# Kernel tuning notes

Hardware: AMD Instinct MI355X
Metric: run time of the kernel (lower is better)

The kernel has to match this reference:

```python
import jax, jax.numpy as jnp
import numpy as np

N, E, G = 50000, 640000, 256
NODE_IN, EDGE_IN, H, L, T = 64, 16, 128, 4, 5
BN_EPS = 1e-5

def setup_inputs() -> dict:
    key = jax.random.key(0)
    ks = jax.random.split(key, 24)
    s = lambda k, shape, fan: jax.random.normal(k, shape, jnp.float32) * (1.0 / np.sqrt(fan))
    return {
        "x": jax.random.normal(ks[0], (N, NODE_IN), jnp.float32),
        "edge_attr": jax.random.normal(ks[1], (E, EDGE_IN), jnp.float32),
        "node_w": s(ks[2], (NODE_IN, H), NODE_IN), "node_b": jnp.zeros((H,), jnp.float32),
        "edge_w1": s(ks[3], (EDGE_IN, H), EDGE_IN), "edge_b1": jnp.zeros((H,), jnp.float32),
        "edge_w2": s(ks[4], (H, H), H), "edge_b2": jnp.zeros((H,), jnp.float32),
        "conv_w1": s(ks[5], (L, H, H), H), "conv_b1": jnp.zeros((L, H), jnp.float32),
        "conv_w2": s(ks[6], (L, H, H), H), "conv_b2": jnp.zeros((L, H), jnp.float32),
        "bn_gamma": jnp.ones((L, H), jnp.float32), "bn_beta": jnp.zeros((L, H), jnp.float32),
        "gate_w1": s(ks[7], (H, H // 2), H), "gate_b1": jnp.zeros((H // 2,), jnp.float32),
        "gate_w2": s(ks[8], (H // 2, 1), H // 2), "gate_b2": jnp.zeros((1,), jnp.float32),
        "head_w1": s(ks[9], (H, H), H), "head_b1": jnp.zeros((H,), jnp.float32),
        "head_w2": s(ks[10], (H, T), H), "head_b2": jnp.zeros((T,), jnp.float32),
        "edge_index": jax.random.randint(ks[11], (2, E), 0, N, jnp.int32),
        "batch": jnp.sort(jax.random.randint(ks[12], (N,), 0, G, jnp.int32)),
    }

def reference(x, edge_attr, node_w, node_b, edge_w1, edge_b1, edge_w2, edge_b2,
              conv_w1, conv_b1, conv_w2, conv_b2, bn_gamma, bn_beta,
              gate_w1, gate_b1, gate_w2, gate_b2, head_w1, head_b1, head_w2, head_b2,
              edge_index, batch):
    relu = jax.nn.relu
    h = x @ node_w + node_b                                   # [N,H]
    e = relu(edge_attr @ edge_w1 + edge_b1) @ edge_w2 + edge_b2  # [E,H]
    src, dst = edge_index[0], edge_index[1]
    bn_scale = 1.0 / jnp.sqrt(jnp.float32(1.0) + BN_EPS)      # eval BN: mean=0, var=1
    for l in range(L):
        m = relu(h[src] + e)                                  # GINEConv message [E,H]
        aggr = jax.ops.segment_sum(m, dst, num_segments=N)    # scatter-add
        z = h + aggr                                          # eps=0: (1+eps)*x + aggr
        z = relu(z @ conv_w1[l] + conv_b1[l]) @ conv_w2[l] + conv_b2[l]
        z = z * bn_scale * bn_gamma[l] + bn_beta[l]
        h = relu(z)                                           # dropout off (eval)
    gate = relu(h @ gate_w1 + gate_b1) @ gate_w2 + gate_b2    # [N,1]
    gmax = jax.ops.segment_max(gate, batch, num_segments=G)   # segment softmax
    wexp = jnp.exp(gate - gmax[batch])
    denom = jax.ops.segment_sum(wexp, batch, num_segments=G)
    alpha = wexp / denom[batch]
    g = jax.ops.segment_sum(alpha * h, batch, num_segments=G) # [G,H]
    return relu(g @ head_w1 + head_b1) @ head_w2 + head_b2    # [G,T]
```

## Files before the change

kernel.cpp:

```cpp
#include <hip/hip_runtime.h>

typedef unsigned short u16;
typedef __bf16 bf16x8 __attribute__((ext_vector_type(8)));
typedef float f32x4 __attribute__((ext_vector_type(4)));
typedef unsigned short u16x8 __attribute__((ext_vector_type(8)));

#define NNODES 50000
#define NEDGES 640000
#define NGRAPH 256

__device__ __forceinline__ float bf2f(u16 u) {
  unsigned int v = ((unsigned int)u) << 16; float f; __builtin_memcpy(&f, &v, 4); return f;
}
__device__ __forceinline__ u16 f2bf(float f) {
  unsigned int x; __builtin_memcpy(&x, &f, 4);
  unsigned int lsb = (x >> 16) & 1u;
  x += 0x7fffu + lsb;
  return (u16)(x >> 16);
}

__global__ void write_zero_f32(float* __restrict__ out, int n) {
  int i = blockIdx.x * 256 + threadIdx.x;
  if (i < n) out[i] = 0.f;
}

__global__ void zero_counts(int* __restrict__ a, int na, int* __restrict__ b, int nb) {
  int i = blockIdx.x * 256 + threadIdx.x;
  if (i < na) a[i] = 0;
  if (i < nb) b[i] = 0;
}

__global__ void prep_weights(const float* __restrict__ node_w, const float* __restrict__ edge_w1,
                             const float* __restrict__ edge_w2, const float* __restrict__ conv_w1,
                             const float* __restrict__ conv_w2, const float* __restrict__ gate_w1,
                             u16* __restrict__ node_wt, u16* __restrict__ edge_w1t,
                             u16* __restrict__ edge_w2t, u16* __restrict__ conv_w1t,
                             u16* __restrict__ conv_w2t, u16* __restrict__ gate_w1t) {
  int o = blockIdx.x * 256 + threadIdx.x;
  if (o < 8192) { int n = o >> 6, k = o & 63; node_wt[o] = f2bf(node_w[k * 128 + n]); return; }
  o -= 8192;
  if (o < 4096) { int n = o >> 5, k = o & 31;
                  edge_w1t[o] = (k < 16) ? f2bf(edge_w1[k * 128 + n]) : (u16)0; return; }
  o -= 4096;
  if (o < 16384) { int n = o >> 7, k = o & 127; edge_w2t[o] = f2bf(edge_w2[k * 128 + n]); return; }
  o -= 16384;
  if (o < 65536) { int l = o >> 14, r = o & 16383, n = r >> 7, k = r & 127;
                   conv_w1t[o] = f2bf(conv_w1[l * 16384 + k * 128 + n]); return; }
  o -= 65536;
  if (o < 65536) { int l = o >> 14, r = o & 16383, n = r >> 7, k = r & 127;
                   conv_w2t[o] = f2bf(conv_w2[l * 16384 + k * 128 + n]); return; }
  o -= 65536;
  if (o < 8192) { int n = o >> 7, k = o & 127; gate_w1t[o] = f2bf(gate_w1[k * 64 + n]); }
}

__global__ void hist_all(const int* __restrict__ dst, const int* __restrict__ b,
                         int* __restrict__ counts, int* __restrict__ gc, int n) {
  int i = blockIdx.x * 256 + threadIdx.x;
  atomicAdd(&counts[dst[i]], 1);
  if (i < n) atomicAdd(&gc[b[i]], 1);
}
__global__ void scan_a(const int* __restrict__ counts, int* __restrict__ bsums, int n) {
  int b = blockIdx.x, t = threadIdx.x;
  int i0 = b * 1024 + t * 4;
  int s = 0;
#pragma unroll
  for (int j = 0; j < 4; j++) { int i = i0 + j; if (i < n) s += counts[i]; }
  int lane = t & 63, w = t >> 6;
  for (int m = 32; m; m >>= 1) s += __shfl_xor(s, m, 64);
  __shared__ int ws_[4];
  if (lane == 0) ws_[w] = s;
  __syncthreads();
  if (t == 0) bsums[b] = ws_[0] + ws_[1] + ws_[2] + ws_[3];
}
__global__ void scan_b(int* __restrict__ bsums, int* __restrict__ offs, int nb, int n) {
  if (threadIdx.x == 0) {
    int run = 0;
    for (int i = 0; i < nb; i++) { int v = bsums[i]; bsums[i] = run; run += v; }
    offs[n] = run;
  }
}
__global__ void scan_c(const int* __restrict__ counts, const int* __restrict__ boffs,
                       int* __restrict__ offs, int* __restrict__ cursor, int n) {
  int b = blockIdx.x, t = threadIdx.x;
  int i0 = b * 1024 + t * 4;
  int v[4]; int s = 0;
#pragma unroll
  for (int j = 0; j < 4; j++) { v[j] = (i0 + j < n) ? counts[i0 + j] : 0; s += v[j]; }
  int lane = t & 63, w = t >> 6;
  int x = s;
  for (int d = 1; d < 64; d <<= 1) { int y = __shfl_up(x, (unsigned)d, 64); if (lane >= d) x += y; }
  __shared__ int wt_[4];
  if (lane == 63) wt_[w] = x;
  __syncthreads();
  int add = boffs[b];
  for (int i = 0; i < w; i++) add += wt_[i];
  int excl = add + x - s;
#pragma unroll
  for (int j = 0; j < 4; j++) {
    int i = i0 + j;
    if (i < n) { offs[i] = excl; cursor[i] = excl; }
    excl += v[j];
  }
}
__global__ void gscan(const int* __restrict__ gcounts, int* __restrict__ goffs) {
  int t = threadIdx.x;
  int v = gcounts[t];
  int lane = t & 63, w = t >> 6;
  int x = v;
  for (int d = 1; d < 64; d <<= 1) { int y = __shfl_up(x, (unsigned)d, 64); if (lane >= d) x += y; }
  __shared__ int wt_[4];
  if (lane == 63) wt_[w] = x;
  __syncthreads();
  int add = 0;
  for (int i = 0; i < w; i++) add += wt_[i];
  int incl = add + x;
  goffs[t] = incl - v;
  if (t == 255) goffs[256] = incl;
}
__global__ void scatter_csr(const int* __restrict__ src, const int* __restrict__ dst,
                            int* __restrict__ cursor, int* __restrict__ csr_src,
                            int* __restrict__ csr_eid) {
  int i = blockIdx.x * 256 + threadIdx.x;
  int d = dst[i];
  int p = atomicAdd(&cursor[d], 1);
  csr_src[p] = src[i];
  csr_eid[p] = i;
}

template <int KB, int SA, int SB>
__device__ __forceinline__ void mfma_block(const u16* aL, const u16* bL, int m, int quad,
                                           int rbase, f32x4* acc) {
#pragma unroll
  for (int kb = 0; kb < KB; ++kb) {
    bf16x8 a = *(const bf16x8*)(aL + (rbase + m) * SA + kb * 32 + quad * 8);
#pragma unroll
    for (int nt = 0; nt < 8; ++nt) {
      bf16x8 b = *(const bf16x8*)(bL + (nt * 16 + m) * SB + kb * 32 + quad * 8);
      acc[nt] = __builtin_amdgcn_mfma_f32_16x16x32_bf16(a, b, acc[nt], 0, 0, 0);
    }
  }
}

__global__ __launch_bounds__(256) void node_encode(const float* __restrict__ x,
                                                   const u16* __restrict__ wt,
                                                   const float* __restrict__ nb,
                                                   u16* __restrict__ hb, int n) {
  __shared__ alignas(16) u16 sA[64 * 72];
  __shared__ alignas(16) u16 sW[128 * 72];
  int t = threadIdx.x;
  int row0 = blockIdx.x * 64;
#pragma unroll
  for (int i = 0; i < 4; i++) {
    int idx = t + 256 * i; int r = idx >> 4, c = idx & 15;
    int grow = row0 + r; if (grow > n - 1) grow = n - 1;
    float4 v = *(const float4*)(x + (size_t)grow * 64 + c * 4);
    ushort4 o; o.x = f2bf(v.x); o.y = f2bf(v.y); o.z = f2bf(v.z); o.w = f2bf(v.w);
    *(ushort4*)&sA[r * 72 + c * 4] = o;
  }
#pragma unroll
  for (int i = 0; i < 4; i++) {
    int idx = t + 256 * i; int nr = idx >> 3, c = idx & 7;
    *(uint4*)&sW[nr * 72 + c * 8] = *(const uint4*)(wt + nr * 64 + c * 8);
  }
  __syncthreads();
  int lane = t & 63, w = t >> 6, m = lane & 15, quad = lane >> 4, rbase = w * 16;
  f32x4 acc[8];
  f32x4 z4 = {0.f, 0.f, 0.f, 0.f};
#pragma unroll
  for (int i = 0; i < 8; i++) acc[i] = z4;
  mfma_block<2, 72, 72>(sA, sW, m, quad, rbase, acc);
#pragma unroll
  for (int nt = 0; nt < 8; nt++) {
    int col = nt * 16 + m;
    float bb = nb[col];
    f32x4 a4 = acc[nt];
#pragma unroll
    for (int r = 0; r < 4; r++) {
      int grow = row0 + rbase + quad * 4 + r;
      if (grow < n) hb[(size_t)grow * 128 + col] = f2bf(a4[r] + bb);
    }
  }
}

__global__ __launch_bounds__(256) void edge_encode(const float* __restrict__ ea,
                                                   const u16* __restrict__ w1t,
                                                   const u16* __restrict__ w2t,
                                                   const float* __restrict__ b1,
                                                   const float* __restrict__ b2,
                                                   const int* __restrict__ csr_eid,
                                                   u16* __restrict__ e_perm) {
  __shared__ alignas(16) u16 sA[64 * 48];
  __shared__ alignas(16) u16 sMid[64 * 136];
  int t = threadIdx.x;
  int lane = t & 63, w = t >> 6, m = lane & 15, quad = lane >> 4, rbase = w * 16;
  int s0 = blockIdx.x * 64;

  if (t < 128) {
    int r = t >> 1, c = t & 1;
    uint4 z = {0, 0, 0, 0};
    *(uint4*)&sA[r * 48 + 16 + c * 8] = z;
  }
  {
    int eidv = 0;
    if (lane < 16) eidv = csr_eid[s0 + w * 16 + lane];
    int r = lane >> 2, c = lane & 3;
    int eid = __shfl(eidv, r, 64);
    float4 v = *(const float4*)(ea + (size_t)eid * 16 + c * 4);
    ushort4 o; o.x = f2bf(v.x); o.y = f2bf(v.y); o.z = f2bf(v.z); o.w = f2bf(v.w);
    *(ushort4*)&sA[(w * 16 + r) * 48 + c * 4] = o;
  }
  bf16x8 w1f[8];
  float b1r[8];
#pragma unroll
  for (int nt = 0; nt < 8; nt++) {
    w1f[nt] = *(const bf16x8*)(w1t + (nt * 16 + m) * 32 + quad * 8);
    b1r[nt] = b1[nt * 16 + m];
  }
  __syncthreads();

  f32x4 z4 = {0.f, 0.f, 0.f, 0.f};
  f32x4 acc[8];
#pragma unroll
  for (int i = 0; i < 8; i++) acc[i] = z4;
  {
    bf16x8 a = *(const bf16x8*)(&sA[(rbase + m) * 48 + quad * 8]);
#pragma unroll
    for (int nt = 0; nt < 8; nt++)
      acc[nt] = __builtin_amdgcn_mfma_f32_16x16x32_bf16(a, w1f[nt], acc[nt], 0, 0, 0);
  }
#pragma unroll
  for (int nt = 0; nt < 8; nt++) {
#pragma unroll
    for (int r = 0; r < 4; r++) {
      float v = fmaxf(acc[nt][r] + b1r[nt], 0.f);
      unsigned int lo = f2bf(v);
      unsigned int hi = __shfl_xor(lo, 1, 64);
      if ((m & 1) == 0) {
        int rr = rbase + quad * 4 + r;
        *(unsigned int*)&sMid[rr * 136 + nt * 16 + m] = lo | (hi << 16);
      }
    }
  }
  bf16x8 w2f[8];
  float4 b2v[2];
#pragma unroll
  for (int ct = 0; ct < 2; ct++) {
    b2v[ct] = *(const float4*)&b2[w * 32 + ct * 16 + quad * 4];
#pragma unroll
    for (int kb = 0; kb < 4; kb++)
      w2f[ct * 4 + kb] = *(const bf16x8*)(w2t + (size_t)(w * 32 + ct * 16 + m) * 128 + kb * 32 + quad * 8);
  }
  __syncthreads();

  f32x4 acc2[8];
#pragma unroll
  for (int i = 0; i < 8; i++) acc2[i] = z4;
#pragma unroll
  for (int rt = 0; rt < 4; rt++) {
#pragma unroll
    for (int kb = 0; kb < 4; kb++) {
      bf16x8 a = *(const bf16x8*)(&sMid[(rt * 16 + m) * 136 + kb * 32 + quad * 8]);
      acc2[rt * 2 + 0] = __builtin_amdgcn_mfma_f32_16x16x32_bf16(w2f[kb], a, acc2[rt * 2 + 0], 0, 0, 0);
      acc2[rt * 2 + 1] = __builtin_amdgcn_mfma_f32_16x16x32_bf16(w2f[4 + kb], a, acc2[rt * 2 + 1], 0, 0, 0);
    }
  }
#pragma unroll
  for (int rt = 0; rt < 4; rt++) {
#pragma unroll
    for (int ct = 0; ct < 2; ct++) {
      f32x4 a4 = acc2[rt * 2 + ct];
      u16 q0 = f2bf(a4[0] + b2v[ct].x);
      u16 q1 = f2bf(a4[1] + b2v[ct].y);
      u16 q2 = f2bf(a4[2] + b2v[ct].z);
      u16 q3 = f2bf(a4[3] + b2v[ct].w);
      uint2 pk;
      pk.x = (unsigned int)q0 | ((unsigned int)q1 << 16);
      pk.y = (unsigned int)q2 | ((unsigned int)q3 << 16);
      *(uint2*)(e_perm + (size_t)(s0 + rt * 16 + m) * 128 + w * 32 + ct * 16 + quad * 4) = pk;
    }
  }
}

__global__ __launch_bounds__(256) void aggregate_k(const u16* __restrict__ hb,
                                                   const u16* __restrict__ e_perm,
                                                   const int* __restrict__ offs,
                                                   const int* __restrict__ csr_src,
                                                   u16* __restrict__ z, int n) {
  int node = blockIdx.x * 4 + (threadIdx.x >> 6);
  if (node >= n) return;
  int lane = threadIdx.x & 63;
  int q = lane >> 4, li = lane & 15;
  int s0 = offs[node], s1 = offs[node + 1];
  float a[8];
#pragma unroll
  for (int j = 0; j < 8; j++) a[j] = 0.f;
  int s = s0 + q;
  for (; s + 8 <= s1; s += 8) {
    int v0 = csr_src[s], v1 = csr_src[s + 4];
    u16x8 h0 = *(const u16x8*)(hb + (size_t)v0 * 128 + li * 8);
    u16x8 e0 = *(const u16x8*)(e_perm + (size_t)s * 128 + li * 8);
    u16x8 h1 = *(const u16x8*)(hb + (size_t)v1 * 128 + li * 8);
    u16x8 e1 = *(const u16x8*)(e_perm + (size_t)(s + 4) * 128 + li * 8);
#pragma unroll
    for (int j = 0; j < 8; j++) {
      a[j] += fmaxf(bf2f(h0[j]) + bf2f(e0[j]), 0.f);
      a[j] += fmaxf(bf2f(h1[j]) + bf2f(e1[j]), 0.f);
    }
  }
  for (; s < s1; s += 4) {
    int v = csr_src[s];
    u16x8 hv = *(const u16x8*)(hb + (size_t)v * 128 + li * 8);
    u16x8 ev = *(const u16x8*)(e_perm + (size_t)s * 128 + li * 8);
#pragma unroll
    for (int j = 0; j < 8; j++) a[j] += fmaxf(bf2f(hv[j]) + bf2f(ev[j]), 0.f);
  }
#pragma unroll
  for (int j = 0; j < 8; j++) {
    a[j] += __shfl_xor(a[j], 16, 64);
    a[j] += __shfl_xor(a[j], 32, 64);
  }
  if (q == 0) {
    u16x8 hv = *(const u16x8*)(hb + (size_t)node * 128 + li * 8);
    u16x8 o;
#pragma unroll
    for (int j = 0; j < 8; j++) o[j] = f2bf(bf2f(hv[j]) + a[j]);
    *(u16x8*)(z + (size_t)node * 128 + li * 8) = o;
  }
}

__global__ __launch_bounds__(256) void conv_mlp(const u16* __restrict__ zb,
                                                u16* __restrict__ hb,
                                                const u16* __restrict__ w1t, const u16* __restrict__ w2t,
                                                const float* __restrict__ b1, const float* __restrict__ b2,
                                                const float* __restrict__ gam, const float* __restrict__ bet,
                                                int n) {
  __shared__ alignas(16) u16 sZ[64 * 136];
  __shared__ alignas(16) u16 sMid[64 * 136];
  int t = threadIdx.x;
  int lane = t & 63, w = t >> 6, m = lane & 15, quad = lane >> 4;
  int row0 = blockIdx.x * 64;
#pragma unroll
  for (int i = 0; i < 4; i++) {
    int idx = t + 256 * i; int r = idx >> 4, c = idx & 15;
    int grow = row0 + r; if (grow > n - 1) grow = n - 1;
    *(uint4*)&sZ[r * 136 + c * 8] = *(const uint4*)(zb + (size_t)grow * 128 + c * 8);
  }
  bf16x8 w1f[8];
  float b1r[2];
#pragma unroll
  for (int ct = 0; ct < 2; ct++) {
    b1r[ct] = b1[w * 32 + ct * 16 + m];
#pragma unroll
    for (int kb = 0; kb < 4; kb++)
      w1f[ct * 4 + kb] = *(const bf16x8*)(w1t + (size_t)(w * 32 + ct * 16 + m) * 128 + kb * 32 + quad * 8);
  }
  __syncthreads();

  f32x4 z4 = {0.f, 0.f, 0.f, 0.f};
  f32x4 acc[8];
#pragma unroll
  for (int i = 0; i < 8; i++) acc[i] = z4;
#pragma unroll
  for (int rt = 0; rt < 4; rt++) {
#pragma unroll
    for (int kb = 0; kb < 4; kb++) {
      bf16x8 a = *(const bf16x8*)(&sZ[(rt * 16 + m) * 136 + kb * 32 + quad * 8]);
      acc[rt * 2 + 0] = __builtin_amdgcn_mfma_f32_16x16x32_bf16(a, w1f[kb], acc[rt * 2 + 0], 0, 0, 0);
      acc[rt * 2 + 1] = __builtin_amdgcn_mfma_f32_16x16x32_bf16(a, w1f[4 + kb], acc[rt * 2 + 1], 0, 0, 0);
    }
  }
#pragma unroll
  for (int rt = 0; rt < 4; rt++) {
#pragma unroll
    for (int ct = 0; ct < 2; ct++) {
#pragma unroll
      for (int r = 0; r < 4; r++) {
        float v = fmaxf(acc[rt * 2 + ct][r] + b1r[ct], 0.f);
        unsigned int lo = f2bf(v);
        unsigned int hi = __shfl_xor(lo, 1, 64);
        if ((m & 1) == 0) {
          int rr = rt * 16 + quad * 4 + r;
          int col = w * 32 + ct * 16 + m;
          *(unsigned int*)&sMid[rr * 136 + col] = lo | (hi << 16);
        }
      }
    }
  }
  bf16x8 w2f[8];
  float4 b2v[2], gamv[2], betv[2];
#pragma unroll
  for (int ct = 0; ct < 2; ct++) {
    int c0 = w * 32 + ct * 16 + quad * 4;
    b2v[ct] = *(const float4*)&b2[c0];
    gamv[ct] = *(const float4*)&gam[c0];
    betv[ct] = *(const float4*)&bet[c0];
#pragma unroll
    for (int kb = 0; kb < 4; kb++)
      w2f[ct * 4 + kb] = *(const bf16x8*)(w2t + (size_t)(w * 32 + ct * 16 + m) * 128 + kb * 32 + quad * 8);
  }
  __syncthreads();

  f32x4 acc2[8];
#pragma unroll
  for (int i = 0; i < 8; i++) acc2[i] = z4;
#pragma unroll
  for (int rt = 0; rt < 4; rt++) {
#pragma unroll
    for (int kb = 0; kb < 4; kb++) {
      bf16x8 a = *(const bf16x8*)(&sMid[(rt * 16 + m) * 136 + kb * 32 + quad * 8]);
      acc2[rt * 2 + 0] = __builtin_amdgcn_mfma_f32_16x16x32_bf16(w2f[kb], a, acc2[rt * 2 + 0], 0, 0, 0);
      acc2[rt * 2 + 1] = __builtin_amdgcn_mfma_f32_16x16x32_bf16(w2f[4 + kb], a, acc2[rt * 2 + 1], 0, 0, 0);
    }
  }
  const float bns = 0.99999500003749983f;
#pragma unroll
  for (int rt = 0; rt < 4; rt++) {
    int grow = row0 + rt * 16 + m;
    if (grow < n) {
#pragma unroll
      for (int ct = 0; ct < 2; ct++) {
        f32x4 a4 = acc2[rt * 2 + ct];
        u16 q0 = f2bf(fmaxf((a4[0] + b2v[ct].x) * bns * gamv[ct].x + betv[ct].x, 0.f));
        u16 q1 = f2bf(fmaxf((a4[1] + b2v[ct].y) * bns * gamv[ct].y + betv[ct].y, 0.f));
        u16 q2 = f2bf(fmaxf((a4[2] + b2v[ct].z) * bns * gamv[ct].z + betv[ct].z, 0.f));
        u16 q3 = f2bf(fmaxf((a4[3] + b2v[ct].w) * bns * gamv[ct].w + betv[ct].w, 0.f));
        uint2 pk;
        pk.x = (unsigned int)q0 | ((unsigned int)q1 << 16);
        pk.y = (unsigned int)q2 | ((unsigned int)q3 << 16);
        *(uint2*)(hb + (size_t)grow * 128 + w * 32 + ct * 16 + quad * 4) = pk;
      }
    }
  }
}

__global__ __launch_bounds__(256) void gate_k(const u16* __restrict__ hb,
                                              const u16* __restrict__ w1t,
                                              const float* __restrict__ b1,
                                              const float* __restrict__ w2,
                                              const float* __restrict__ b2,
                                              float* __restrict__ gate, int n) {
  __shared__ alignas(16) u16 sA[64 * 136];
  __shared__ alignas(16) u16 sW[64 * 136];
  int t = threadIdx.x;
  int row0 = blockIdx.x * 64;
#pragma unroll
  for (int i = 0; i < 4; i++) {
    int idx = t + 256 * i; int r = idx >> 4, c = idx & 15;
    int grow = row0 + r; if (grow > n - 1) grow = n - 1;
    *(uint4*)&sA[r * 136 + c * 8] = *(const uint4*)(hb + (size_t)grow * 128 + c * 8);
  }
#pragma unroll
  for (int i = 0; i < 4; i++) {
    int idx = t + 256 * i; int r = idx >> 4, c = idx & 15;
    *(uint4*)&sW[r * 136 + c * 8] = *(const uint4*)(w1t + r * 128 + c * 8);
  }
  __syncthreads();
  int lane = t & 63, w = t >> 6, m = lane & 15, quad = lane >> 4, rbase = w * 16;
  f32x4 z4 = {0.f, 0.f, 0.f, 0.f};
  f32x4 acc[4];
#pragma unroll
  for (int i = 0; i < 4; i++) acc[i] = z4;
#pragma unroll
  for (int kb = 0; kb < 4; kb++) {
    bf16x8 a = *(const bf16x8*)(&sA[(rbase + m) * 136 + kb * 32 + quad * 8]);
#pragma unroll
    for (int nt = 0; nt < 4; nt++) {
      bf16x8 b = *(const bf16x8*)(&sW[(nt * 16 + m) * 136 + kb * 32 + quad * 8]);
      acc[nt] = __builtin_amdgcn_mfma_f32_16x16x32_bf16(a, b, acc[nt], 0, 0, 0);
    }
  }
  float b1v[4], w2v[4];
#pragma unroll
  for (int nt = 0; nt < 4; nt++) { b1v[nt] = b1[nt * 16 + m]; w2v[nt] = w2[nt * 16 + m]; }
  float b2v = b2[0];
#pragma unroll
  for (int r = 0; r < 4; r++) {
    float p = 0.f;
#pragma unroll
    for (int nt = 0; nt < 4; nt++) p += fmaxf(acc[nt][r] + b1v[nt], 0.f) * w2v[nt];
    p += __shfl_xor(p, 1, 64);
    p += __shfl_xor(p, 2, 64);
    p += __shfl_xor(p, 4, 64);
    p += __shfl_xor(p, 8, 64);
    if (m == 0) {
      int grow = row0 + rbase + quad * 4 + r;
      if (grow < n) gate[grow] = p + b2v;
    }
  }
}

__global__ __launch_bounds__(256) void pool_k(const float* __restrict__ gate,
                                              const u16* __restrict__ hb,
                                              const int* __restrict__ goffs,
                                              float* __restrict__ gpool) {
  int g = blockIdx.x, t = threadIdx.x;
  int s0 = goffs[g], s1 = goffs[g + 1];
  int lane = t & 63, w = t >> 6;
  __shared__ float red[4];
  __shared__ float fin[2][128];
  float mx = -3.4e38f;
  for (int i = s0 + t; i < s1; i += 256) mx = fmaxf(mx, gate[i]);
  for (int d = 32; d; d >>= 1) mx = fmaxf(mx, __shfl_xor(mx, d, 64));
  if (lane == 0) red[w] = mx;
  __syncthreads();
  mx = fmaxf(fmaxf(red[0], red[1]), fmaxf(red[2], red[3]));
  __syncthreads();
  float sm = 0.f;
  for (int i = s0 + t; i < s1; i += 256) sm += __expf(gate[i] - mx);
  for (int d = 32; d; d >>= 1) sm += __shfl_xor(sm, d, 64);
  if (lane == 0) red[w] = sm;
  __syncthreads();
  sm = red[0] + red[1] + red[2] + red[3];
  int g2 = t >> 7, tc = t & 127;
  float acc = 0.f;
  for (int i = s0 + g2; i < s1; i += 2)
    acc += __expf(gate[i] - mx) * bf2f(hb[(size_t)i * 128 + tc]);
  fin[g2][tc] = acc;
  __syncthreads();
  if (t < 128) gpool[g * 128 + t] = (s1 > s0) ? (fin[0][t] + fin[1][t]) / sm : 0.f;
}

__global__ __launch_bounds__(128) void head_k(const float* __restrict__ gpool,
                                              const float* __restrict__ w1, const float* __restrict__ b1,
                                              const float* __restrict__ w2, const float* __restrict__ b2,
                                              float* __restrict__ out) {
  int g = blockIdx.x, t = threadIdx.x;
  __shared__ float sg[128];
  __shared__ float shid[128];
  sg[t] = gpool[g * 128 + t];
  __syncthreads();
  float s = 0.f;
  for (int k = 0; k < 128; k++) s += sg[k] * w1[k * 128 + t];
  shid[t] = fmaxf(s + b1[t], 0.f);
  __syncthreads();
  if (t < 5) {
    float o = b2[t];
    for (int k = 0; k < 128; k++) o += shid[k] * w2[k * 5 + t];
    out[g * 5 + t] = o;
  }
}

extern "C" void kernel_launch(void* const* d_in, const int* in_sizes, int n_in,
                              void* d_out, int out_size, void* d_ws, size_t ws_size,
                              hipStream_t stream) {
  const int N = NNODES, E = NEDGES, G = NGRAPH;
  const float* x = (const float*)d_in[0];
  const float* edge_attr = (const float*)d_in[1];
  const float* node_w = (const float*)d_in[2];
  const float* node_b = (const float*)d_in[3];
  const float* edge_w1 = (const float*)d_in[4];
  const float* edge_b1 = (const float*)d_in[5];
  const float* edge_w2 = (const float*)d_in[6];
  const float* edge_b2 = (const float*)d_in[7];
  const float* conv_w1 = (const float*)d_in[8];
  const float* conv_b1 = (const float*)d_in[9];
  const float* conv_w2 = (const float*)d_in[10];
  const float* conv_b2 = (const float*)d_in[11];
  const float* bn_gamma = (const float*)d_in[12];
  const float* bn_beta = (const float*)d_in[13];
  const float* gate_w1 = (const float*)d_in[14];
  const float* gate_b1 = (const float*)d_in[15];
  const float* gate_w2 = (const float*)d_in[16];
  const float* gate_b2 = (const float*)d_in[17];
  const float* head_w1 = (const float*)d_in[18];
  const float* head_b1 = (const float*)d_in[19];
  const float* head_w2 = (const float*)d_in[20];
  const float* head_b2 = (const float*)d_in[21];
  const int* eidx = (const int*)d_in[22];
  const int* batch = (const int*)d_in[23];
  const int* esrc = eidx;
  const int* edst = eidx + E;

  char* wp = (char*)d_ws;
  auto alloc = [&](size_t bytes) { char* p = wp; wp += (bytes + 255) & ~(size_t)255; return p; };
  u16* e_perm = (u16*)alloc((size_t)E * 128 * 2);
  u16* hb = (u16*)alloc((size_t)(N + 16) * 128 * 2);
  u16* zb = (u16*)alloc((size_t)N * 128 * 2);
  float* gate = (float*)alloc((size_t)N * 4);
  float* gpool = (float*)alloc((size_t)G * 128 * 4);
  int* counts = (int*)alloc((size_t)N * 4);
  int* offs = (int*)alloc((size_t)(N + 1) * 4);
  int* cursor = (int*)alloc((size_t)N * 4);
  int* csr_src = (int*)alloc((size_t)E * 4);
  int* csr_eid = (int*)alloc((size_t)E * 4);
  int* bsums = (int*)alloc(64 * 4);
  int* gcounts = (int*)alloc(G * 4);
  int* goffs = (int*)alloc((G + 1) * 4);
  u16* node_wt = (u16*)alloc(8192 * 2);
  u16* edge_w1t = (u16*)alloc(4096 * 2);
  u16* edge_w2t = (u16*)alloc(16384 * 2);
  u16* conv_w1t = (u16*)alloc(65536 * 2);
  u16* conv_w2t = (u16*)alloc(65536 * 2);
  u16* gate_w1t = (u16*)alloc(8192 * 2);

  size_t need = (size_t)(wp - (char*)d_ws);
  if (need > ws_size) {
    write_zero_f32<<<(out_size + 255) / 256, 256, 0, stream>>>((float*)d_out, out_size);
    return;
  }

  zero_counts<<<(N + 255) / 256, 256, 0, stream>>>(counts, N, gcounts, G);
  prep_weights<<<656, 256, 0, stream>>>(node_w, edge_w1, edge_w2, conv_w1, conv_w2, gate_w1,
                                        node_wt, edge_w1t, edge_w2t, conv_w1t, conv_w2t, gate_w1t);
  hist_all<<<E / 256, 256, 0, stream>>>(edst, batch, counts, gcounts, N);
  scan_a<<<49, 256, 0, stream>>>(counts, bsums, N);
  scan_b<<<1, 64, 0, stream>>>(bsums, offs, 49, N);
  scan_c<<<49, 256, 0, stream>>>(counts, bsums, offs, cursor, N);
  gscan<<<1, 256, 0, stream>>>(gcounts, goffs);
  scatter_csr<<<E / 256, 256, 0, stream>>>(esrc, edst, cursor, csr_src, csr_eid);
  node_encode<<<(N + 63) / 64, 256, 0, stream>>>(x, node_wt, node_b, hb, N);
  edge_encode<<<E / 64, 256, 0, stream>>>(edge_attr, edge_w1t, edge_w2t, edge_b1, edge_b2,
                                          csr_eid, e_perm);
  for (int l = 0; l < 4; l++) {
    aggregate_k<<<(N + 3) / 4, 256, 0, stream>>>(hb, e_perm, offs, csr_src, zb, N);
    conv_mlp<<<(N + 63) / 64, 256, 0, stream>>>(zb, hb, conv_w1t + l * 16384, conv_w2t + l * 16384,
                                                conv_b1 + l * 128, conv_b2 + l * 128,
                                                bn_gamma + l * 128, bn_beta + l * 128, N);
  }
  gate_k<<<(N + 63) / 64, 256, 0, stream>>>(hb, gate_w1t, gate_b1, gate_w2, gate_b2, gate, N);
  pool_k<<<G, 256, 0, stream>>>(gate, hb, goffs, gpool);
  head_k<<<G, 128, 0, stream>>>(gpool, head_w1, head_b1, head_w2, head_b2, (float*)d_out);
}
```

Baseline: 687.9 us.

## Fuse neighbor aggregation into conv MLP kernel with ping-pong node buffers

Merges the per-layer aggregation kernel into the conv MLP kernel. Each block gathers the CSR neighbors for its 64 nodes straight into shared memory and then runs the two matmuls. Node features ping-pong between two buffers, which removes the z round trip through global memory and one launch per layer. The MFMA operand order is swapped so the bias/ReLU epilogue writes packed 4-wide values without shuffles, and outputs are staged through LDS for coalesced stores in both edge_encode and layer_k. The cost is lower gather parallelism: each 16-lane group now processes 4 nodes serially, versus 4 nodes per 64-thread block before, which risks worse latency hiding on the irregular gathers.

```diff
diff --git a/kernel.cpp b/kernel.cpp
--- a/kernel.cpp
+++ b/kernel.cpp
@@ -210,12 +210,9 @@
     *(ushort4*)&sA[(w * 16 + r) * 48 + c * 4] = o;
   }
   bf16x8 w1f[8];
-  float b1r[8];
-#pragma unroll
-  for (int nt = 0; nt < 8; nt++) {
+#pragma unroll
+  for (int nt = 0; nt < 8; nt++)
     w1f[nt] = *(const bf16x8*)(w1t + (nt * 16 + m) * 32 + quad * 8);
-    b1r[nt] = b1[nt * 16 + m];
-  }
   __syncthreads();
 
   f32x4 z4 = {0.f, 0.f, 0.f, 0.f};
@@ -226,20 +223,19 @@
     bf16x8 a = *(const bf16x8*)(&sA[(rbase + m) * 48 + quad * 8]);
 #pragma unroll
     for (int nt = 0; nt < 8; nt++)
-      acc[nt] = __builtin_amdgcn_mfma_f32_16x16x32_bf16(a, w1f[nt], acc[nt], 0, 0, 0);
+      acc[nt] = __builtin_amdgcn_mfma_f32_16x16x32_bf16(w1f[nt], a, acc[nt], 0, 0, 0);
   }
 #pragma unroll
   for (int nt = 0; nt < 8; nt++) {
-#pragma unroll
-    for (int r = 0; r < 4; r++) {
-      float v = fmaxf(acc[nt][r] + b1r[nt], 0.f);
-      unsigned int lo = f2bf(v);
-      unsigned int hi = __shfl_xor(lo, 1, 64);
-      if ((m & 1) == 0) {
-        int rr = rbase + quad * 4 + r;
-        *(unsigned int*)&sMid[rr * 136 + nt * 16 + m] = lo | (hi << 16);
-      }
-    }
+    float4 bb = *(const float4*)&b1[nt * 16 + quad * 4];
+    u16 q0 = f2bf(fmaxf(acc[nt][0] + bb.x, 0.f));
+    u16 q1 = f2bf(fmaxf(acc[nt][1] + bb.y, 0.f));
+    u16 q2 = f2bf(fmaxf(acc[nt][2] + bb.z, 0.f));
+    u16 q3 = f2bf(fmaxf(acc[nt][3] + bb.w, 0.f));
+    uint2 pk;
+    pk.x = (unsigned int)q0 | ((unsigned int)q1 << 16);
+    pk.y = (unsigned int)q2 | ((unsigned int)q3 << 16);
+    *(uint2*)&sMid[(rbase + m) * 136 + nt * 16 + quad * 4] = pk;
   }
   bf16x8 w2f[8];
   float4 b2v[2];
@@ -264,6 +260,7 @@
       acc2[rt * 2 + 1] = __builtin_amdgcn_mfma_f32_16x16x32_bf16(w2f[4 + kb], a, acc2[rt * 2 + 1], 0, 0, 0);
     }
   }
+  __syncthreads();
 #pragma unroll
   for (int rt = 0; rt < 4; rt++) {
 #pragma unroll
@@ -276,80 +273,72 @@
       uint2 pk;
       pk.x = (unsigned int)q0 | ((unsigned int)q1 << 16);
       pk.y = (unsigned int)q2 | ((unsigned int)q3 << 16);
-      *(uint2*)(e_perm + (size_t)(s0 + rt * 16 + m) * 128 + w * 32 + ct * 16 + quad * 4) = pk;
-    }
-  }
-}
-
-__global__ __launch_bounds__(256) void aggregate_k(const u16* __restrict__ hb,
-                                                   const u16* __restrict__ e_perm,
-                                                   const int* __restrict__ offs,
-                                                   const int* __restrict__ csr_src,
-                                                   u16* __restrict__ z, int n) {
-  int node = blockIdx.x * 4 + (threadIdx.x >> 6);
-  if (node >= n) return;
-  int lane = threadIdx.x & 63;
-  int q = lane >> 4, li = lane & 15;
-  int s0 = offs[node], s1 = offs[node + 1];
-  float a[8];
-#pragma unroll
-  for (int j = 0; j < 8; j++) a[j] = 0.f;
-  int s = s0 + q;
-  for (; s + 8 <= s1; s += 8) {
-    int v0 = csr_src[s], v1 = csr_src[s + 4];
-    u16x8 h0 = *(const u16x8*)(hb + (size_t)v0 * 128 + li * 8);
-    u16x8 e0 = *(const u16x8*)(e_perm + (size_t)s * 128 + li * 8);
-    u16x8 h1 = *(const u16x8*)(hb + (size_t)v1 * 128 + li * 8);
-    u16x8 e1 = *(const u16x8*)(e_perm + (size_t)(s + 4) * 128 + li * 8);
-#pragma unroll
-    for (int j = 0; j < 8; j++) {
-      a[j] += fmaxf(bf2f(h0[j]) + bf2f(e0[j]), 0.f);
-      a[j] += fmaxf(bf2f(h1[j]) + bf2f(e1[j]), 0.f);
-    }
-  }
-  for (; s < s1; s += 4) {
-    int v = csr_src[s];
-    u16x8 hv = *(const u16x8*)(hb + (size_t)v * 128 + li * 8);
-    u16x8 ev = *(const u16x8*)(e_perm + (size_t)s * 128 + li * 8);
-#pragma unroll
-    for (int j = 0; j < 8; j++) a[j] += fmaxf(bf2f(hv[j]) + bf2f(ev[j]), 0.f);
-  }
-#pragma unroll
-  for (int j = 0; j < 8; j++) {
-    a[j] += __shfl_xor(a[j], 16, 64);
-    a[j] += __shfl_xor(a[j], 32, 64);
-  }
-  if (q == 0) {
-    u16x8 hv = *(const u16x8*)(hb + (size_t)node * 128 + li * 8);
-    u16x8 o;
-#pragma unroll
-    for (int j = 0; j < 8; j++) o[j] = f2bf(bf2f(hv[j]) + a[j]);
-    *(u16x8*)(z + (size_t)node * 128 + li * 8) = o;
-  }
-}
-
-__global__ __launch_bounds__(256) void conv_mlp(const u16* __restrict__ zb,
-                                                u16* __restrict__ hb,
-                                                const u16* __restrict__ w1t, const u16* __restrict__ w2t,
-                                                const float* __restrict__ b1, const float* __restrict__ b2,
-                                                const float* __restrict__ gam, const float* __restrict__ bet,
-                                                int n) {
+      *(uint2*)&sMid[(rt * 16 + m) * 136 + w * 32 + ct * 16 + quad * 4] = pk;
+    }
+  }
+  __syncthreads();
+#pragma unroll
+  for (int i = 0; i < 4; i++) {
+    int idx = t + 256 * i; int r = idx >> 4, c = idx & 15;
+    *(uint4*)(e_perm + (size_t)(s0 + r) * 128 + c * 8) = *(const uint4*)&sMid[r * 136 + c * 8];
+  }
+}
+
+__global__ __launch_bounds__(256) void layer_k(const u16* __restrict__ hin,
+                                               u16* __restrict__ hout,
+                                               const u16* __restrict__ e_perm,
+                                               const int* __restrict__ offs,
+                                               const int* __restrict__ csr_src,
+                                               const u16* __restrict__ w1t, const u16* __restrict__ w2t,
+                                               const float* __restrict__ b1, const float* __restrict__ b2,
+                                               const float* __restrict__ gam, const float* __restrict__ bet,
+                                               int n) {
   __shared__ alignas(16) u16 sZ[64 * 136];
   __shared__ alignas(16) u16 sMid[64 * 136];
   int t = threadIdx.x;
   int lane = t & 63, w = t >> 6, m = lane & 15, quad = lane >> 4;
   int row0 = blockIdx.x * 64;
-#pragma unroll
-  for (int i = 0; i < 4; i++) {
-    int idx = t + 256 * i; int r = idx >> 4, c = idx & 15;
-    int grow = row0 + r; if (grow > n - 1) grow = n - 1;
-    *(uint4*)&sZ[r * 136 + c * 8] = *(const uint4*)(zb + (size_t)grow * 128 + c * 8);
+  int li = m;
+  int qq = w * 4 + quad;
+
+  for (int k = 0; k < 4; k++) {
+    int lr = qq * 4 + k;
+    int nd = row0 + lr; if (nd > n - 1) nd = n - 1;
+    int s0 = offs[nd], s1 = offs[nd + 1];
+    float a[8];
+#pragma unroll
+    for (int j = 0; j < 8; j++) a[j] = 0.f;
+    int s = s0;
+    for (; s + 2 <= s1; s += 2) {
+      int v0 = csr_src[s], v1 = csr_src[s + 1];
+      u16x8 h0 = *(const u16x8*)(hin + (size_t)v0 * 128 + li * 8);
+      u16x8 e0 = *(const u16x8*)(e_perm + (size_t)s * 128 + li * 8);
+      u16x8 h1 = *(const u16x8*)(hin + (size_t)v1 * 128 + li * 8);
+      u16x8 e1 = *(const u16x8*)(e_perm + (size_t)(s + 1) * 128 + li * 8);
+#pragma unroll
+      for (int j = 0; j < 8; j++) {
+        a[j] += fmaxf(bf2f(h0[j]) + bf2f(e0[j]), 0.f);
+        a[j] += fmaxf(bf2f(h1[j]) + bf2f(e1[j]), 0.f);
+      }
+    }
+    if (s < s1) {
+      int v = csr_src[s];
+      u16x8 hv = *(const u16x8*)(hin + (size_t)v * 128 + li * 8);
+      u16x8 ev = *(const u16x8*)(e_perm + (size_t)s * 128 + li * 8);
+#pragma unroll
+      for (int j = 0; j < 8; j++) a[j] += fmaxf(bf2f(hv[j]) + bf2f(ev[j]), 0.f);
+    }
+    u16x8 hv = *(const u16x8*)(hin + (size_t)nd * 128 + li * 8);
+    u16x8 o;
+#pragma unroll
+    for (int j = 0; j < 8; j++) o[j] = f2bf(bf2f(hv[j]) + a[j]);
+    *(u16x8*)&sZ[lr * 136 + li * 8] = o;
   }
   bf16x8 w1f[8];
-  float b1r[2];
+  float4 b1v[2];
 #pragma unroll
   for (int ct = 0; ct < 2; ct++) {
-    b1r[ct] = b1[w * 32 + ct * 16 + m];
+    b1v[ct] = *(const float4*)&b1[w * 32 + ct * 16 + quad * 4];
 #pragma unroll
     for (int kb = 0; kb < 4; kb++)
       w1f[ct * 4 + kb] = *(const bf16x8*)(w1t + (size_t)(w * 32 + ct * 16 + m) * 128 + kb * 32 + quad * 8);
@@ -365,25 +354,23 @@
 #pragma unroll
     for (int kb = 0; kb < 4; kb++) {
       bf16x8 a = *(const bf16x8*)(&sZ[(rt * 16 + m) * 136 + kb * 32 + quad * 8]);
-      acc[rt * 2 + 0] = __builtin_amdgcn_mfma_f32_16x16x32_bf16(a, w1f[kb], acc[rt * 2 + 0], 0, 0, 0);
-      acc[rt * 2 + 1] = __builtin_amdgcn_mfma_f32_16x16x32_bf16(a, w1f[4 + kb], acc[rt * 2 + 1], 0, 0, 0);
+      acc[rt * 2 + 0] = __builtin_amdgcn_mfma_f32_16x16x32_bf16(w1f[kb], a, acc[rt * 2 + 0], 0, 0, 0);
+      acc[rt * 2 + 1] = __builtin_amdgcn_mfma_f32_16x16x32_bf16(w1f[4 + kb], a, acc[rt * 2 + 1], 0, 0, 0);
     }
   }
 #pragma unroll
   for (int rt = 0; rt < 4; rt++) {
 #pragma unroll
     for (int ct = 0; ct < 2; ct++) {
-#pragma unroll
-      for (int r = 0; r < 4; r++) {
-        float v = fmaxf(acc[rt * 2 + ct][r] + b1r[ct], 0.f);
-        unsigned int lo = f2bf(v);
-        unsigned int hi = __shfl_xor(lo, 1, 64);
-        if ((m & 1) == 0) {
-          int rr = rt * 16 + quad * 4 + r;
-          int col = w * 32 + ct * 16 + m;
-          *(unsigned int*)&sMid[rr * 136 + col] = lo | (hi << 16);
-        }
-      }
+      f32x4 a4 = acc[rt * 2 + ct];
+      u16 q0 = f2bf(fmaxf(a4[0] + b1v[ct].x, 0.f));
+      u16 q1 = f2bf(fmaxf(a4[1] + b1v[ct].y, 0.f));
+      u16 q2 = f2bf(fmaxf(a4[2] + b1v[ct].z, 0.f));
+      u16 q3 = f2bf(fmaxf(a4[3] + b1v[ct].w, 0.f));
+      uint2 pk;
+      pk.x = (unsigned int)q0 | ((unsigned int)q1 << 16);
+      pk.y = (unsigned int)q2 | ((unsigned int)q3 << 16);
+      *(uint2*)&sMid[(rt * 16 + m) * 136 + w * 32 + ct * 16 + quad * 4] = pk;
     }
   }
   bf16x8 w2f[8];
@@ -415,21 +402,26 @@
   const float bns = 0.99999500003749983f;
 #pragma unroll
   for (int rt = 0; rt < 4; rt++) {
-    int grow = row0 + rt * 16 + m;
-    if (grow < n) {
-#pragma unroll
-      for (int ct = 0; ct < 2; ct++) {
-        f32x4 a4 = acc2[rt * 2 + ct];
-        u16 q0 = f2bf(fmaxf((a4[0] + b2v[ct].x) * bns * gamv[ct].x + betv[ct].x, 0.f));
-        u16 q1 = f2bf(fmaxf((a4[1] + b2v[ct].y) * bns * gamv[ct].y + betv[ct].y, 0.f));
-        u16 q2 = f2bf(fmaxf((a4[2] + b2v[ct].z) * bns * gamv[ct].z + betv[ct].z, 0.f));
-        u16 q3 = f2bf(fmaxf((a4[3] + b2v[ct].w) * bns * gamv[ct].w + betv[ct].w, 0.f));
-        uint2 pk;
-        pk.x = (unsigned int)q0 | ((unsigned int)q1 << 16);
-        pk.y = (unsigned int)q2 | ((unsigned int)q3 << 16);
-        *(uint2*)(hb + (size_t)grow * 128 + w * 32 + ct * 16 + quad * 4) = pk;
-      }
-    }
+#pragma unroll
+    for (int ct = 0; ct < 2; ct++) {
+      f32x4 a4 = acc2[rt * 2 + ct];
+      u16 q0 = f2bf(fmaxf((a4[0] + b2v[ct].x) * bns * gamv[ct].x + betv[ct].x, 0.f));
+      u16 q1 = f2bf(fmaxf((a4[1] + b2v[ct].y) * bns * gamv[ct].y + betv[ct].y, 0.f));
+      u16 q2 = f2bf(fmaxf((a4[2] + b2v[ct].z) * bns * gamv[ct].z + betv[ct].z, 0.f));
+      u16 q3 = f2bf(fmaxf((a4[3] + b2v[ct].w) * bns * gamv[ct].w + betv[ct].w, 0.f));
+      uint2 pk;
+      pk.x = (unsigned int)q0 | ((unsigned int)q1 << 16);
+      pk.y = (unsigned int)q2 | ((unsigned int)q3 << 16);
+      *(uint2*)&sZ[(rt * 16 + m) * 136 + w * 32 + ct * 16 + quad * 4] = pk;
+    }
+  }
+  __syncthreads();
+#pragma unroll
+  for (int i = 0; i < 4; i++) {
+    int idx = t + 256 * i; int r = idx >> 4, c = idx & 15;
+    int grow = row0 + r;
+    if (grow < n)
+      *(uint4*)(hout + (size_t)grow * 128 + c * 8) = *(const uint4*)&sZ[r * 136 + c * 8];
   }
 }
 
@@ -575,7 +567,7 @@
   auto alloc = [&](size_t bytes) { char* p = wp; wp += (bytes + 255) & ~(size_t)255; return p; };
   u16* e_perm = (u16*)alloc((size_t)E * 128 * 2);
   u16* hb = (u16*)alloc((size_t)(N + 16) * 128 * 2);
-  u16* zb = (u16*)alloc((size_t)N * 128 * 2);
+  u16* hb2 = (u16*)alloc((size_t)(N + 16) * 128 * 2);
   float* gate = (float*)alloc((size_t)N * 4);
   float* gpool = (float*)alloc((size_t)G * 128 * 4);
   int* counts = (int*)alloc((size_t)N * 4);
@@ -611,13 +603,16 @@
   node_encode<<<(N + 63) / 64, 256, 0, stream>>>(x, node_wt, node_b, hb, N);
   edge_encode<<<E / 64, 256, 0, stream>>>(edge_attr, edge_w1t, edge_w2t, edge_b1, edge_b2,
                                           csr_eid, e_perm);
+  u16* hcur = hb;
+  u16* hnext = hb2;
   for (int l = 0; l < 4; l++) {
-    aggregate_k<<<(N + 3) / 4, 256, 0, stream>>>(hb, e_perm, offs, csr_src, zb, N);
-    conv_mlp<<<(N + 63) / 64, 256, 0, stream>>>(zb, hb, conv_w1t + l * 16384, conv_w2t + l * 16384,
-                                                conv_b1 + l * 128, conv_b2 + l * 128,
-                                                bn_gamma + l * 128, bn_beta + l * 128, N);
-  }
-  gate_k<<<(N + 63) / 64, 256, 0, stream>>>(hb, gate_w1t, gate_b1, gate_w2, gate_b2, gate, N);
-  pool_k<<<G, 256, 0, stream>>>(gate, hb, goffs, gpool);
+    layer_k<<<(N + 63) / 64, 256, 0, stream>>>(hcur, hnext, e_perm, offs, csr_src,
+                                               conv_w1t + l * 16384, conv_w2t + l * 16384,
+                                               conv_b1 + l * 128, conv_b2 + l * 128,
+                                               bn_gamma + l * 128, bn_beta + l * 128, N);
+    u16* tmp = hcur; hcur = hnext; hnext = tmp;
+  }
+  gate_k<<<(N + 63) / 64, 256, 0, stream>>>(hcur, gate_w1t, gate_b1, gate_w2, gate_b2, gate, N);
+  pool_k<<<G, 256, 0, stream>>>(gate, hcur, goffs, gpool);
   head_k<<<G, 128, 0, stream>>>(gpool, head_w1, head_b1, head_w2, head_b2, (float*)d_out);
 }
```

After: 655.2 us. -4.7%, faster.
